# Kernel tuning notes

Hardware: AMD Instinct MI355X
Metric: run time of the kernel (lower is better)

The kernel has to match this reference:

```python
import jax, jax.numpy as jnp
import numpy as np

EMBED_DIM = 512
NUM_HEADS = 8
HEAD_DIM = EMBED_DIM // NUM_HEADS


def setup_inputs() -> dict:
    key = jax.random.key(0)
    k1, k2, kw, kb, kow, kob = jax.random.split(key, 6)
    B, L, C = 2, 2048, EMBED_DIM
    s = 1.0 / np.sqrt(C)
    return {
        "x1": jax.random.normal(k1, (B, L, C), dtype=jnp.float32),
        "x2": jax.random.normal(k2, (B, L, C), dtype=jnp.float32),
        # nn.Linear(embed_dim, 3*embed_dim): weight [3C, C], bias [3C]
        "qkv_w": jax.random.uniform(kw, (3 * C, C), jnp.float32, -s, s),
        "qkv_b": jax.random.uniform(kb, (3 * C,), jnp.float32, -s, s),
        # nn.Linear(embed_dim, embed_dim): weight [C, C], bias [C]
        "out_w": jax.random.uniform(kow, (C, C), jnp.float32, -s, s),
        "out_b": jax.random.uniform(kob, (C,), jnp.float32, -s, s),
    }


def _qkv(x, qkv_w, qkv_b):
    B, L, C = x.shape
    H, D = NUM_HEADS, C // NUM_HEADS
    # Linear: x @ W^T + b, then view(B, L, H, 3, D) and split along the '3' axis
    qkv = (jnp.einsum("blc,fc->blf", x, qkv_w) + qkv_b).reshape(B, L, H, 3, D)
    qkv = jnp.transpose(qkv, (3, 0, 2, 1, 4))  # [3, B, H, L, D]
    return qkv[0], qkv[1], qkv[2]


def _attend(q, k, v):
    # q,k,v: [B, H, L, D]; scale by 1/sqrt(D)
    scale = 1.0 / np.sqrt(q.shape[-1]).astype(np.float32)
    scores = jnp.einsum("bhqd,bhkd->bhqk", q, k) * scale  # [B,H,L,L]
    attn = jax.nn.softmax(scores, axis=-1)
    out = jnp.einsum("bhqk,bhkd->bhqd", attn, v)
    B, H, L, D = out.shape
    return jnp.transpose(out, (0, 2, 1, 3)).reshape(B, L, H * D)


def reference(x1, x2, qkv_w, qkv_b, out_w, out_b):
    q1, k1, v1 = _qkv(x1, qkv_w, qkv_b)
    q2, k2, v2 = _qkv(x2, qkv_w, qkv_b)
    out1 = _attend(q1, k2, v2)  # q from x1, k/v from x2
    out2 = _attend(q2, k1, v1)  # q from x2, k/v from x1
    out1 = jnp.einsum("blc,fc->blf", out1, out_w) + out_b
    out2 = jnp.einsum("blc,fc->blf", out2, out_w) + out_b
    return (out1, out2)
```

## Files before the change

kernel.cpp:

```cpp
#include <hip/hip_runtime.h>
#include <stdint.h>

typedef unsigned short u16;
typedef unsigned int u32;
typedef short bf16x8 __attribute__((ext_vector_type(8)));
typedef float f32x4 __attribute__((ext_vector_type(4)));
typedef float f32x16 __attribute__((ext_vector_type(16)));

#define K_DIM 512

__device__ __forceinline__ u16 f2bf(float f) {
  union { float f; u32 u; } v; v.f = f;
  return (u16)((v.u + 0x8000u) >> 16);
}
__device__ __forceinline__ u32 pk2(float lo, float hi) {
  union { float f; u32 u; } a, b; a.f = lo; b.f = hi;
  return __builtin_amdgcn_perm(b.u + 0x8000u, a.u + 0x8000u, 0x07060302u);
}

__global__ void cvt_kernel(const float* __restrict__ x1, const float* __restrict__ x2,
                           const float* __restrict__ qkvw, const float* __restrict__ outw,
                           u16* __restrict__ xb, u16* __restrict__ wqkv, u16* __restrict__ wout) {
  int tid = blockIdx.x * 256 + threadIdx.x;
  const float4* src; u16* dst; int idx = tid;
  if (idx < 524288)        { src = (const float4*)x1;   dst = xb; }
  else if (idx < 1048576)  { src = (const float4*)x2;   dst = xb + 2097152; idx -= 524288; }
  else if (idx < 1245184)  { src = (const float4*)qkvw; dst = wqkv;         idx -= 1048576; }
  else                     { src = (const float4*)outw; dst = wout;         idx -= 1245184; }
  float4 v = src[idx];
  *(uint2*)&dst[idx * 4] = make_uint2(pk2(v.x, v.y), pk2(v.z, v.w));
}

#define LDA 40

__global__ __launch_bounds__(256, 3) void qkv_gemm(
    const u16* __restrict__ A, const u16* __restrict__ W, const float* __restrict__ bias,
    u16* __restrict__ qb, u16* __restrict__ kb, u16* __restrict__ vtb) {
  __shared__ __align__(16) u16 As[2][128 * LDA];
  __shared__ __align__(16) u16 Bs[2][128 * LDA];
  const int t = threadIdx.x;
  const int m0 = blockIdx.x * 128, n0 = blockIdx.y * 128;
  const int lane = t & 63, l16 = lane & 15, quad = lane >> 4;
  const int w = t >> 6;
  const int wm = (w >> 1) * 64, wn = (w & 1) * 64;
  const int sr = t >> 2, sc = (t & 3) * 8;

  const u16* Ap = A + (size_t)(m0 + sr) * K_DIM + sc;
  const u16* Wp = W + (size_t)(n0 + sr) * K_DIM + sc;

  f32x4 acc[4][4];
#pragma unroll
  for (int i = 0; i < 4; ++i)
#pragma unroll
    for (int j = 0; j < 4; ++j) acc[i][j] = (f32x4){0.f, 0.f, 0.f, 0.f};

  uint4 ra0 = *(const uint4*)(Ap);
  uint4 ra1 = *(const uint4*)(Ap + 64 * K_DIM);
  uint4 rb0 = *(const uint4*)(Wp);
  uint4 rb1 = *(const uint4*)(Wp + 64 * K_DIM);
  *(uint4*)&As[0][sr * LDA + sc] = ra0;
  *(uint4*)&As[0][(sr + 64) * LDA + sc] = ra1;
  *(uint4*)&Bs[0][sr * LDA + sc] = rb0;
  *(uint4*)&Bs[0][(sr + 64) * LDA + sc] = rb1;
  ra0 = *(const uint4*)(Ap + 32);
  ra1 = *(const uint4*)(Ap + 64 * K_DIM + 32);
  rb0 = *(const uint4*)(Wp + 32);
  rb1 = *(const uint4*)(Wp + 64 * K_DIM + 32);
  __syncthreads();

  for (int kt = 0; kt < 16; ++kt) {
    const int cur = kt & 1, nxt = cur ^ 1;
    if (kt < 15) {
      *(uint4*)&As[nxt][sr * LDA + sc] = ra0;
      *(uint4*)&As[nxt][(sr + 64) * LDA + sc] = ra1;
      *(uint4*)&Bs[nxt][sr * LDA + sc] = rb0;
      *(uint4*)&Bs[nxt][(sr + 64) * LDA + sc] = rb1;
    }
    if (kt < 14) {
      int ko = (kt + 2) * 32;
      ra0 = *(const uint4*)(Ap + ko);
      ra1 = *(const uint4*)(Ap + 64 * K_DIM + ko);
      rb0 = *(const uint4*)(Wp + ko);
      rb1 = *(const uint4*)(Wp + 64 * K_DIM + ko);
    }
    bf16x8 af[4], bfr[4];
#pragma unroll
    for (int mi = 0; mi < 4; ++mi)
      af[mi] = *(const bf16x8*)&As[cur][(wm + mi * 16 + l16) * LDA + quad * 8];
#pragma unroll
    for (int ni = 0; ni < 4; ++ni)
      bfr[ni] = *(const bf16x8*)&Bs[cur][(wn + ni * 16 + l16) * LDA + quad * 8];
#pragma unroll
    for (int mi = 0; mi < 4; ++mi)
#pragma unroll
      for (int ni = 0; ni < 4; ++ni)
        acc[mi][ni] = __builtin_amdgcn_mfma_f32_16x16x32_bf16(bfr[ni], af[mi], acc[mi][ni], 0, 0, 0);
    __syncthreads();
  }

  const int fbase = n0 + wn;
  const int h = fbase / 192;
  const int s = (fbase - h * 192) >> 6;
  float4 bv[4];
#pragma unroll
  for (int ni = 0; ni < 4; ++ni)
    bv[ni] = *(const float4*)&bias[fbase + ni * 16 + quad * 4];
  const int bh = m0 >> 11;
  const int lbase = (m0 & 2047) + wm;

  if (s == 2) {
    u16* dst = vtb + (size_t)((bh * 8 + h) * 64) * 2048;
#pragma unroll
    for (int mi = 0; mi < 4; ++mi) {
      int l = lbase + mi * 16 + l16;
#pragma unroll
      for (int ni = 0; ni < 4; ++ni)
#pragma unroll
        for (int r = 0; r < 4; ++r)
          dst[(ni * 16 + quad * 4 + r) * 2048 + l] = f2bf(acc[mi][ni][r] + bv[ni][r]);
    }
  } else {
    u16* dst = (s == 0 ? qb : kb) + (size_t)((bh * 8 + h) * 2048) * 64;
    const float sc2 = (s == 0) ? 0.18033688011112042f : 1.0f;
#pragma unroll
    for (int mi = 0; mi < 4; ++mi) {
      int l = lbase + mi * 16 + l16;
#pragma unroll
      for (int ni = 0; ni < 4; ++ni) {
        float v0 = (acc[mi][ni][0] + bv[ni][0]) * sc2;
        float v1 = (acc[mi][ni][1] + bv[ni][1]) * sc2;
        float v2 = (acc[mi][ni][2] + bv[ni][2]) * sc2;
        float v3 = (acc[mi][ni][3] + bv[ni][3]) * sc2;
        *(uint2*)&dst[(size_t)l * 64 + ni * 16 + quad * 4] = make_uint2(pk2(v0, v1), pk2(v2, v3));
      }
    }
  }
}

#define LQ 72

#define SPHASE(SS, KBUF)                                                          \
  do {                                                                            \
    _Pragma("unroll") for (int r_ = 0; r_ < 16; ++r_) {                           \
      SS[0][r_] = 0.f; SS[1][r_] = 0.f;                                           \
    }                                                                             \
    _Pragma("unroll") for (int ks_ = 0; ks_ < 4; ++ks_) {                         \
      bf16x8 kfr0 = *(const bf16x8*)&Ks[KBUF][l32 * LQ + ks_ * 16 + h2 * 8];      \
      bf16x8 kfr1 = *(const bf16x8*)&Ks[KBUF][(32 + l32) * LQ + ks_ * 16 + h2 * 8]; \
      SS[0] = __builtin_amdgcn_mfma_f32_32x32x16_bf16(kfr0, qf[ks_], SS[0], 0, 0, 0); \
      SS[1] = __builtin_amdgcn_mfma_f32_32x32x16_bf16(kfr1, qf[ks_], SS[1], 0, 0, 0); \
    }                                                                             \
  } while (0)

#define SOFTPV(SS, VBUF)                                                          \
  do {                                                                            \
    bf16x8 pf[4];                                                                 \
    _Pragma("unroll") for (int mi_ = 0; mi_ < 2; ++mi_) {                         \
      float p[16];                                                                \
      _Pragma("unroll") for (int r_ = 0; r_ < 16; ++r_)                           \
        p[r_] = __builtin_amdgcn_exp2f(SS[mi_][r_]);                              \
      _Pragma("unroll") for (int r_ = 0; r_ < 16; r_ += 4)                        \
        rs += (p[r_] + p[r_ + 1]) + (p[r_ + 2] + p[r_ + 3]);                      \
      u32 a0 = pk2(p[0], p[1]),   b0 = pk2(p[2], p[3]);                           \
      u32 c0 = pk2(p[4], p[5]),   d0 = pk2(p[6], p[7]);                           \
      u32 a1 = pk2(p[8], p[9]),   b1 = pk2(p[10], p[11]);                         \
      u32 c1 = pk2(p[12], p[13]), d1 = pk2(p[14], p[15]);                         \
      asm("v_permlane32_swap_b32 %0, %1" : "+v"(a0), "+v"(c0));                   \
      asm("v_permlane32_swap_b32 %0, %1" : "+v"(b0), "+v"(d0));                   \
      asm("v_permlane32_swap_b32 %0, %1" : "+v"(a1), "+v"(c1));                   \
      asm("v_permlane32_swap_b32 %0, %1" : "+v"(b1), "+v"(d1));                   \
      union { u32 u[4]; bf16x8 v; } f0_, f1_;                                     \
      f0_.u[0] = a0; f0_.u[1] = b0; f0_.u[2] = c0; f0_.u[3] = d0;                 \
      f1_.u[0] = a1; f1_.u[1] = b1; f1_.u[2] = c1; f1_.u[3] = d1;                 \
      pf[mi_ * 2] = f0_.v; pf[mi_ * 2 + 1] = f1_.v;                               \
    }                                                                             \
    const u16* vb_ = (const u16*)VTs + (VBUF) * (64 * LQ);                        \
    _Pragma("unroll") for (int ks_ = 0; ks_ < 4; ++ks_) {                         \
      bf16x8 vf0 = *(const bf16x8*)&vb_[l32 * LQ + ks_ * 16 + h2 * 8];            \
      bf16x8 vf1 = *(const bf16x8*)&vb_[(32 + l32) * LQ + ks_ * 16 + h2 * 8];     \
      oacc[0] = __builtin_amdgcn_mfma_f32_32x32x16_bf16(vf0, pf[ks_], oacc[0], 0, 0, 0); \
      oacc[1] = __builtin_amdgcn_mfma_f32_32x32x16_bf16(vf1, pf[ks_], oacc[1], 0, 0, 0); \
    }                                                                             \
  } while (0)

__global__ __launch_bounds__(256, 2) void attn_kernel(
    const u16* __restrict__ qb, const u16* __restrict__ kb, const u16* __restrict__ vtb,
    u16* __restrict__ attnb) {
  __shared__ __align__(16) u16 Ks[2][64 * LQ];
  __shared__ __align__(16) u16 VTs[4][64 * LQ];

  const int t = threadIdx.x;
  const int w = t >> 6, lane = t & 63, l32 = lane & 31, h2 = lane >> 5;
  const int bid = blockIdx.x;
  const int comb = bid & 31;
  const int qt = bid >> 5;
  const int h = comb & 7, bb = (comb >> 3) & 1, pair = comb >> 4;
  const int in_q = pair, in_kv = pair ^ 1;

  const u16* Qg = qb + (size_t)((in_q * 2 + bb) * 8 + h) * 2048 * 64;
  const u16* Kg = kb + (size_t)((in_kv * 2 + bb) * 8 + h) * 2048 * 64;
  const u16* Vg = vtb + (size_t)((in_kv * 2 + bb) * 8 + h) * 64 * 2048;

  const int srow = t >> 3, sseg = (t & 7) * 8;
  uint4 rk0 = *(const uint4*)(Kg + srow * 64 + sseg);
  uint4 rk1 = *(const uint4*)(Kg + (srow + 32) * 64 + sseg);
  uint4 rv0 = *(const uint4*)(Vg + srow * 2048 + sseg);
  uint4 rv1 = *(const uint4*)(Vg + (srow + 32) * 2048 + sseg);

  bf16x8 qf[4];
#pragma unroll
  for (int ks = 0; ks < 4; ++ks)
    qf[ks] = *(const bf16x8*)(Qg + (qt * 128 + w * 32 + l32) * 64 + ks * 16 + h2 * 8);

  auto stage = [&](int kbuf, int vbuf) {
    *(uint4*)&Ks[kbuf][srow * LQ + sseg] = rk0;
    *(uint4*)&Ks[kbuf][(srow + 32) * LQ + sseg] = rk1;
    *(uint4*)&VTs[vbuf][srow * LQ + sseg] = rv0;
    *(uint4*)&VTs[vbuf][(srow + 32) * LQ + sseg] = rv1;
  };
  auto gload = [&](int kt) {
    const int ko = kt * 64;
    rk0 = *(const uint4*)(Kg + (ko + srow) * 64 + sseg);
    rk1 = *(const uint4*)(Kg + (ko + srow + 32) * 64 + sseg);
    rv0 = *(const uint4*)(Vg + srow * 2048 + ko + sseg);
    rv1 = *(const uint4*)(Vg + (srow + 32) * 2048 + ko + sseg);
  };

  f32x16 oacc[2];
#pragma unroll
  for (int mi = 0; mi < 2; ++mi)
#pragma unroll
    for (int r = 0; r < 16; ++r) oacc[mi][r] = 0.f;
  float rs = 0.f;
  f32x16 sA, sB;
  f32x16 sAa[2], sBa[2];
#pragma unroll
  for (int r = 0; r < 16; ++r) { sAa[0][r] = 0.f; sAa[1][r] = 0.f; sBa[0][r] = 0.f; sBa[1][r] = 0.f; }

  stage(0, 0);
  gload(1);
  __syncthreads();

  stage(1, 1);
  gload(2);
  SPHASE(sAa, 0);
  __syncthreads();

#pragma unroll 1
  for (int it = 0; it < 16; ++it) {
    const int e = (it & 1) << 1;
    if (it < 15) {
      stage(0, e ^ 2);
      gload(2 * it + 3);
    }
    SPHASE(sBa, 1);
    SOFTPV(sAa, e);
    if (it == 15) break;
    __syncthreads();
    stage(1, e ^ 3);
    if (it < 14) gload(2 * it + 4);
    SPHASE(sAa, 0);
    SOFTPV(sBa, e + 1);
    __syncthreads();
  }
  SOFTPV(sBa, 3);

  rs += __shfl_xor(rs, 32);
  const float inv = 1.0f / rs;
  const int row = in_q * 4096 + bb * 2048 + qt * 128 + w * 32 + l32;
#pragma unroll
  for (int mi = 0; mi < 2; ++mi)
#pragma unroll
    for (int rg = 0; rg < 4; ++rg) {
      float v0 = oacc[mi][rg * 4 + 0] * inv;
      float v1 = oacc[mi][rg * 4 + 1] * inv;
      float v2 = oacc[mi][rg * 4 + 2] * inv;
      float v3 = oacc[mi][rg * 4 + 3] * inv;
      *(uint2*)&attnb[(size_t)row * 512 + h * 64 + mi * 32 + rg * 8 + h2 * 4] =
          make_uint2(pk2(v0, v1), pk2(v2, v3));
    }
}

__global__ __launch_bounds__(256, 2) void out_gemm(
    const u16* __restrict__ A, const u16* __restrict__ W, const float* __restrict__ bias,
    float* __restrict__ out) {
  __shared__ __align__(16) u16 As[2][64 * LDA];
  __shared__ __align__(16) u16 Bs[2][128 * LDA];
  const int t = threadIdx.x;
  const int m0 = blockIdx.x * 64, n0 = blockIdx.y * 128;
  const int lane = t & 63, l16 = lane & 15, quad = lane >> 4;
  const int w = t >> 6;
  const int wm = (w & 1) * 32, wn = (w >> 1) * 64;
  const int ar = t >> 2, ac = (t & 3) * 8;
  const int sr = t >> 2, sc = (t & 3) * 8;

  const u16* Ap = A + (size_t)(m0 + ar) * K_DIM + ac;
  const u16* Wp = W + (size_t)(n0 + sr) * K_DIM + sc;

  f32x4 acc[2][4];
#pragma unroll
  for (int i = 0; i < 2; ++i)
#pragma unroll
    for (int j = 0; j < 4; ++j) acc[i][j] = (f32x4){0.f, 0.f, 0.f, 0.f};

  uint4 ra = *(const uint4*)Ap;
  uint4 rb0 = *(const uint4*)(Wp);
  uint4 rb1 = *(const uint4*)(Wp + 64 * K_DIM);
  *(uint4*)&As[0][ar * LDA + ac] = ra;
  *(uint4*)&Bs[0][sr * LDA + sc] = rb0;
  *(uint4*)&Bs[0][(sr + 64) * LDA + sc] = rb1;
  ra = *(const uint4*)(Ap + 32);
  rb0 = *(const uint4*)(Wp + 32);
  rb1 = *(const uint4*)(Wp + 64 * K_DIM + 32);
  __syncthreads();

  for (int kt = 0; kt < 16; ++kt) {
    const int cur = kt & 1, nxt = cur ^ 1;
    if (kt < 15) {
      *(uint4*)&As[nxt][ar * LDA + ac] = ra;
      *(uint4*)&Bs[nxt][sr * LDA + sc] = rb0;
      *(uint4*)&Bs[nxt][(sr + 64) * LDA + sc] = rb1;
    }
    if (kt < 14) {
      int ko = (kt + 2) * 32;
      ra = *(const uint4*)(Ap + ko);
      rb0 = *(const uint4*)(Wp + ko);
      rb1 = *(const uint4*)(Wp + 64 * K_DIM + ko);
    }
    bf16x8 af[2], bfr[4];
#pragma unroll
    for (int mi = 0; mi < 2; ++mi)
      af[mi] = *(const bf16x8*)&As[cur][(wm + mi * 16 + l16) * LDA + quad * 8];
#pragma unroll
    for (int ni = 0; ni < 4; ++ni)
      bfr[ni] = *(const bf16x8*)&Bs[cur][(wn + ni * 16 + l16) * LDA + quad * 8];
#pragma unroll
    for (int mi = 0; mi < 2; ++mi)
#pragma unroll
      for (int ni = 0; ni < 4; ++ni)
        acc[mi][ni] = __builtin_amdgcn_mfma_f32_16x16x32_bf16(af[mi], bfr[ni], acc[mi][ni], 0, 0, 0);
    __syncthreads();
  }

#pragma unroll
  for (int ni = 0; ni < 4; ++ni) {
    int f = n0 + wn + ni * 16 + l16;
    float bv = bias[f];
#pragma unroll
    for (int mi = 0; mi < 2; ++mi)
#pragma unroll
      for (int r = 0; r < 4; ++r) {
        int m = m0 + wm + mi * 16 + quad * 4 + r;
        out[(size_t)m * 512 + f] = acc[mi][ni][r] + bv;
      }
  }
}

extern "C" void kernel_launch(void* const* d_in, const int* in_sizes, int n_in,
                              void* d_out, int out_size, void* d_ws, size_t ws_size,
                              hipStream_t stream) {
  const float* x1   = (const float*)d_in[0];
  const float* x2   = (const float*)d_in[1];
  const float* qkvw = (const float*)d_in[2];
  const float* qkvb = (const float*)d_in[3];
  const float* outw = (const float*)d_in[4];
  const float* outb = (const float*)d_in[5];
  float* out = (float*)d_out;
  char* ws = (char*)d_ws;

  u16* xb    = (u16*)(ws + 0);
  u16* wqkv  = (u16*)(ws + 8388608);
  u16* wout  = (u16*)(ws + 9961472);
  u16* qb    = (u16*)(ws + 10485760);
  u16* kb    = (u16*)(ws + 18874368);
  u16* vtb   = (u16*)(ws + 27262976);
  u16* attnb = (u16*)(ws + 0);

  cvt_kernel<<<5120, 256, 0, stream>>>(x1, x2, qkvw, outw, xb, wqkv, wout);

  dim3 g1(64, 12);
  qkv_gemm<<<g1, 256, 0, stream>>>(xb, wqkv, qkvb, qb, kb, vtb);

  attn_kernel<<<512, 256, 0, stream>>>(qb, kb, vtb, attnb);

  dim3 g3(128, 4);
  out_gemm<<<g3, 256, 0, stream>>>(attnb, wout, outb, out);
}
```

Baseline: 153.6 us.

## Use direct global-to-LDS loads with XOR-swizzled tiles in projection GEMMs

The QKV and output projection GEMMs now use global_load_lds to copy tiles straight into shared memory instead of staging them through registers and storing them with ds_write. The padded LDA=40 layout is replaced by an unpadded 32-wide layout with an XOR swizzle on 16-byte chunks, applied on both the load side and the fragment-read side, to avoid bank conflicts. This cuts register pressure and VALU/LDS store instructions, but prefetch depth drops from two tiles in flight to one. Correctness relies on the swizzle and per-wave LDS destination mapping lining up.

Measured after the change: 152.7 us. Within noise of the previous version (-0.6%).

```diff
diff --git a/kernel.cpp b/kernel.cpp
--- a/kernel.cpp
+++ b/kernel.cpp
@@ -8,6 +8,9 @@
 typedef float f32x16 __attribute__((ext_vector_type(16)));
 
 #define K_DIM 512
+
+typedef __attribute__((address_space(1))) const unsigned char gls_g;
+typedef __attribute__((address_space(3))) unsigned char gls_s;
 
 __device__ __forceinline__ u16 f2bf(float f) {
   union { float f; u32 u; } v; v.f = f;
@@ -31,22 +34,30 @@
   *(uint2*)&dst[idx * 4] = make_uint2(pk2(v.x, v.y), pk2(v.z, v.w));
 }
 
-#define LDA 40
-
 __global__ __launch_bounds__(256, 3) void qkv_gemm(
     const u16* __restrict__ A, const u16* __restrict__ W, const float* __restrict__ bias,
     u16* __restrict__ qb, u16* __restrict__ kb, u16* __restrict__ vtb) {
-  __shared__ __align__(16) u16 As[2][128 * LDA];
-  __shared__ __align__(16) u16 Bs[2][128 * LDA];
+  __shared__ __align__(16) u16 As[2][128 * 32];
+  __shared__ __align__(16) u16 Bs[2][128 * 32];
   const int t = threadIdx.x;
   const int m0 = blockIdx.x * 128, n0 = blockIdx.y * 128;
   const int lane = t & 63, l16 = lane & 15, quad = lane >> 4;
   const int w = t >> 6;
   const int wm = (w >> 1) * 64, wn = (w & 1) * 64;
-  const int sr = t >> 2, sc = (t & 3) * 8;
-
-  const u16* Ap = A + (size_t)(m0 + sr) * K_DIM + sc;
-  const u16* Wp = W + (size_t)(n0 + sr) * K_DIM + sc;
+
+  const int gchunk = (lane & 3) ^ ((lane >> 3) & 3);
+  const int grow = w * 32 + (lane >> 2);
+  const u16* Ag = A + (size_t)(m0 + grow) * K_DIM + gchunk * 8;
+  const u16* Wg = W + (size_t)(n0 + grow) * K_DIM + gchunk * 8;
+  const int swz = (quad ^ ((l16 >> 1) & 3)) << 3;
+
+  auto gll = [&](int buf, int kt) {
+    const int ko = kt * 32;
+    __builtin_amdgcn_global_load_lds((gls_g*)(Ag + ko), (gls_s*)&As[buf][w * 1024], 16, 0, 0);
+    __builtin_amdgcn_global_load_lds((gls_g*)(Ag + 16 * K_DIM + ko), (gls_s*)&As[buf][w * 1024 + 512], 16, 0, 0);
+    __builtin_amdgcn_global_load_lds((gls_g*)(Wg + ko), (gls_s*)&Bs[buf][w * 1024], 16, 0, 0);
+    __builtin_amdgcn_global_load_lds((gls_g*)(Wg + 16 * K_DIM + ko), (gls_s*)&Bs[buf][w * 1024 + 512], 16, 0, 0);
+  };
 
   f32x4 acc[4][4];
 #pragma unroll
@@ -54,42 +65,19 @@
 #pragma unroll
     for (int j = 0; j < 4; ++j) acc[i][j] = (f32x4){0.f, 0.f, 0.f, 0.f};
 
-  uint4 ra0 = *(const uint4*)(Ap);
-  uint4 ra1 = *(const uint4*)(Ap + 64 * K_DIM);
-  uint4 rb0 = *(const uint4*)(Wp);
-  uint4 rb1 = *(const uint4*)(Wp + 64 * K_DIM);
-  *(uint4*)&As[0][sr * LDA + sc] = ra0;
-  *(uint4*)&As[0][(sr + 64) * LDA + sc] = ra1;
-  *(uint4*)&Bs[0][sr * LDA + sc] = rb0;
-  *(uint4*)&Bs[0][(sr + 64) * LDA + sc] = rb1;
-  ra0 = *(const uint4*)(Ap + 32);
-  ra1 = *(const uint4*)(Ap + 64 * K_DIM + 32);
-  rb0 = *(const uint4*)(Wp + 32);
-  rb1 = *(const uint4*)(Wp + 64 * K_DIM + 32);
+  gll(0, 0);
   __syncthreads();
 
   for (int kt = 0; kt < 16; ++kt) {
     const int cur = kt & 1, nxt = cur ^ 1;
-    if (kt < 15) {
-      *(uint4*)&As[nxt][sr * LDA + sc] = ra0;
-      *(uint4*)&As[nxt][(sr + 64) * LDA + sc] = ra1;
-      *(uint4*)&Bs[nxt][sr * LDA + sc] = rb0;
-      *(uint4*)&Bs[nxt][(sr + 64) * LDA + sc] = rb1;
-    }
-    if (kt < 14) {
-      int ko = (kt + 2) * 32;
-      ra0 = *(const uint4*)(Ap + ko);
-      ra1 = *(const uint4*)(Ap + 64 * K_DIM + ko);
-      rb0 = *(const uint4*)(Wp + ko);
-      rb1 = *(const uint4*)(Wp + 64 * K_DIM + ko);
-    }
+    if (kt < 15) gll(nxt, kt + 1);
     bf16x8 af[4], bfr[4];
 #pragma unroll
     for (int mi = 0; mi < 4; ++mi)
-      af[mi] = *(const bf16x8*)&As[cur][(wm + mi * 16 + l16) * LDA + quad * 8];
+      af[mi] = *(const bf16x8*)&As[cur][(wm + mi * 16 + l16) * 32 + swz];
 #pragma unroll
     for (int ni = 0; ni < 4; ++ni)
-      bfr[ni] = *(const bf16x8*)&Bs[cur][(wn + ni * 16 + l16) * LDA + quad * 8];
+      bfr[ni] = *(const bf16x8*)&Bs[cur][(wn + ni * 16 + l16) * 32 + swz];
 #pragma unroll
     for (int mi = 0; mi < 4; ++mi)
 #pragma unroll
@@ -232,7 +220,6 @@
 #pragma unroll
     for (int r = 0; r < 16; ++r) oacc[mi][r] = 0.f;
   float rs = 0.f;
-  f32x16 sA, sB;
   f32x16 sAa[2], sBa[2];
 #pragma unroll
   for (int r = 0; r < 16; ++r) { sAa[0][r] = 0.f; sAa[1][r] = 0.f; sBa[0][r] = 0.f; sBa[1][r] = 0.f; }
@@ -284,18 +271,25 @@
 __global__ __launch_bounds__(256, 2) void out_gemm(
     const u16* __restrict__ A, const u16* __restrict__ W, const float* __restrict__ bias,
     float* __restrict__ out) {
-  __shared__ __align__(16) u16 As[2][64 * LDA];
-  __shared__ __align__(16) u16 Bs[2][128 * LDA];
+  __shared__ __align__(16) u16 As[2][64 * 32];
+  __shared__ __align__(16) u16 Bs[2][128 * 32];
   const int t = threadIdx.x;
   const int m0 = blockIdx.x * 64, n0 = blockIdx.y * 128;
   const int lane = t & 63, l16 = lane & 15, quad = lane >> 4;
   const int w = t >> 6;
   const int wm = (w & 1) * 32, wn = (w >> 1) * 64;
-  const int ar = t >> 2, ac = (t & 3) * 8;
-  const int sr = t >> 2, sc = (t & 3) * 8;
-
-  const u16* Ap = A + (size_t)(m0 + ar) * K_DIM + ac;
-  const u16* Wp = W + (size_t)(n0 + sr) * K_DIM + sc;
+
+  const int gchunk = (lane & 3) ^ ((lane >> 3) & 3);
+  const u16* Ag = A + (size_t)(m0 + w * 16 + (lane >> 2)) * K_DIM + gchunk * 8;
+  const u16* Wg = W + (size_t)(n0 + w * 32 + (lane >> 2)) * K_DIM + gchunk * 8;
+  const int swz = (quad ^ ((l16 >> 1) & 3)) << 3;
+
+  auto gll = [&](int buf, int kt) {
+    const int ko = kt * 32;
+    __builtin_amdgcn_global_load_lds((gls_g*)(Ag + ko), (gls_s*)&As[buf][w * 512], 16, 0, 0);
+    __builtin_amdgcn_global_load_lds((gls_g*)(Wg + ko), (gls_s*)&Bs[buf][w * 1024], 16, 0, 0);
+    __builtin_amdgcn_global_load_lds((gls_g*)(Wg + 16 * K_DIM + ko), (gls_s*)&Bs[buf][w * 1024 + 512], 16, 0, 0);
+  };
 
   f32x4 acc[2][4];
 #pragma unroll
@@ -303,37 +297,19 @@
 #pragma unroll
     for (int j = 0; j < 4; ++j) acc[i][j] = (f32x4){0.f, 0.f, 0.f, 0.f};
 
-  uint4 ra = *(const uint4*)Ap;
-  uint4 rb0 = *(const uint4*)(Wp);
-  uint4 rb1 = *(const uint4*)(Wp + 64 * K_DIM);
-  *(uint4*)&As[0][ar * LDA + ac] = ra;
-  *(uint4*)&Bs[0][sr * LDA + sc] = rb0;
-  *(uint4*)&Bs[0][(sr + 64) * LDA + sc] = rb1;
-  ra = *(const uint4*)(Ap + 32);
-  rb0 = *(const uint4*)(Wp + 32);
-  rb1 = *(const uint4*)(Wp + 64 * K_DIM + 32);
+  gll(0, 0);
   __syncthreads();
 
   for (int kt = 0; kt < 16; ++kt) {
     const int cur = kt & 1, nxt = cur ^ 1;
-    if (kt < 15) {
-      *(uint4*)&As[nxt][ar * LDA + ac] = ra;
-      *(uint4*)&Bs[nxt][sr * LDA + sc] = rb0;
-      *(uint4*)&Bs[nxt][(sr + 64) * LDA + sc] = rb1;
-    }
-    if (kt < 14) {
-      int ko = (kt + 2) * 32;
-      ra = *(const uint4*)(Ap + ko);
-      rb0 = *(const uint4*)(Wp + ko);
-      rb1 = *(const uint4*)(Wp + 64 * K_DIM + ko);
-    }
+    if (kt < 15) gll(nxt, kt + 1);
     bf16x8 af[2], bfr[4];
 #pragma unroll
     for (int mi = 0; mi < 2; ++mi)
-      af[mi] = *(const bf16x8*)&As[cur][(wm + mi * 16 + l16) * LDA + quad * 8];
+      af[mi] = *(const bf16x8*)&As[cur][(wm + mi * 16 + l16) * 32 + swz];
 #pragma unroll
     for (int ni = 0; ni < 4; ++ni)
-      bfr[ni] = *(const bf16x8*)&Bs[cur][(wn + ni * 16 + l16) * LDA + quad * 8];
+      bfr[ni] = *(const bf16x8*)&Bs[cur][(wn + ni * 16 + l16) * 32 + swz];
 #pragma unroll
     for (int mi = 0; mi < 2; ++mi)
 #pragma unroll
```
